# Performance work log

Hardware: AMD Instinct MI355X
Metric: run time of the kernel (lower is better)

Reference implementation:

```python
import jax, jax.numpy as jnp
import numpy as np

N = 100_000      # number of sparse voxels / points
M = 1_000_000    # number of kernel-map (key,query) pairs
C_IN = 128
C_OUT = 128
H = 8            # num_heads
CH = C_OUT // H  # attn_channels = 16
KVOL = 27        # kernel_volume for kernel_size=3, dim=3
EPS_BN = 1e-5
EPS_NORM = 1e-12


def _bn(x, gamma, beta):
    # BatchNorm1d in training mode: batch statistics over point dim
    mu = jnp.mean(x, axis=0)
    var = jnp.var(x, axis=0)
    return (x - mu) * jax.lax.rsqrt(var + EPS_BN) * gamma + beta


def _l2norm(x):
    # F.normalize(p=2, dim=-1) with eps clamp
    n = jnp.sqrt(jnp.sum(x * x, axis=-1, keepdims=True))
    return x / jnp.maximum(n, EPS_NORM)


def setup_inputs() -> dict:
    key = jax.random.key(0)
    ks = jax.random.split(key, 14)
    inp = {
        "points": jax.random.normal(ks[0], (N, 3), jnp.float32),
        "feats": jax.random.normal(ks[1], (N, C_IN), jnp.float32),
        "k_idx": jax.random.randint(ks[2], (M,), 0, N),
        "q_idx": jax.random.randint(ks[3], (M,), 0, N),
        "kernel_idx": jax.random.randint(ks[4], (M,), 0, KVOL),
        # intra_pos_mlp params: Linear(3,3,no bias)-BN-ReLU-Linear(3,C_IN,no bias)-BN-ReLU-Linear(C_IN,C_IN)
        "w1": jax.random.normal(ks[5], (3, 3), jnp.float32) / np.float32(np.sqrt(3.0)),
        "g1": jnp.ones((3,), jnp.float32),
        "b1": jnp.zeros((3,), jnp.float32),
        "w2": jax.random.normal(ks[6], (3, C_IN), jnp.float32) / np.float32(np.sqrt(3.0)),
        "g2": jnp.ones((C_IN,), jnp.float32),
        "b2": jnp.zeros((C_IN,), jnp.float32),
        "w3": jax.random.normal(ks[7], (C_IN, C_IN), jnp.float32) / np.float32(np.sqrt(C_IN)),
        "b3": jnp.zeros((C_IN,), jnp.float32),
        # to_query / to_value (1x1 Minkowski conv == per-point linear) and to_out
        "wq": jax.random.normal(ks[8], (C_IN, C_OUT), jnp.float32) / np.float32(np.sqrt(C_IN)),
        "bq": jnp.zeros((C_OUT,), jnp.float32),
        "wv": jax.random.normal(ks[9], (C_IN, C_OUT), jnp.float32) / np.float32(np.sqrt(C_IN)),
        "bv": jnp.zeros((C_OUT,), jnp.float32),
        "wo": jax.random.normal(ks[10], (C_OUT, C_OUT), jnp.float32) / np.float32(np.sqrt(C_OUT)),
        "bo": jnp.zeros((C_OUT,), jnp.float32),
        # inter_pos_enc ~ N(0,1) per nn.init.normal_
        "pos_enc": jax.random.normal(ks[11], (KVOL, H, CH), jnp.float32),
    }
    return inp


def reference(points, feats, k_idx, q_idx, kernel_idx,
              w1, g1, b1, w2, g2, b2, w3, b3,
              wq, bq, wv, bv, wo, bo, pos_enc):
    # intra positional encoding MLP, added to features
    h = jax.nn.relu(_bn(points @ w1, g1, b1))
    h = jax.nn.relu(_bn(h @ w2, g2, b2))
    x = feats + (h @ w3 + b3)                       # [N, C_IN]
    # per-point query / value projections
    q = (x @ wq + bq).reshape(N, H, CH)             # [N, H, CH]
    v = (x @ wv + bv).reshape(N, H, CH)
    qn = _l2norm(q)
    pn = _l2norm(pos_enc)                           # [KVOL, H, CH]
    # DotProduct op: attn[m,h] = <norm_q[q_idx[m],h], norm_pos_enc[kernel_idx[m],h]>
    attn = jnp.einsum('mhc,mhc->mh', qn[q_idx], pn[kernel_idx])  # [M, H]
    # ScalarAttention op: out[q_idx[m],h,:] += attn[m,h] * v[k_idx[m],h,:]
    out = jnp.zeros((N, H, CH), feats.dtype).at[q_idx].add(attn[:, :, None] * v[k_idx])
    # to_out linear
    return out.reshape(N, C_OUT) @ wo + bo          # [N, C_OUT]
```

## Files before the change

### kernel.cpp

```cpp
#include <hip/hip_runtime.h>
#include <hip/hip_bf16.h>

#define CIN 128
#define NHEAD 8
#define CHD 16
#define KVOL 27
#define NBKT_MAX 512
#define CH 4096
#define NB1 64
#define NB2 256

constexpr float EPS_BN = 1e-5f;
constexpr float EPS_NORM = 1e-12f;

typedef __attribute__((ext_vector_type(8))) short short8;
typedef __attribute__((ext_vector_type(4))) float f32x4;

__device__ __forceinline__ float bflo(unsigned u) {
  return __uint_as_float(u << 16);
}
__device__ __forceinline__ float bfhi(unsigned u) {
  return __uint_as_float(u & 0xffff0000u);
}
__device__ __forceinline__ unsigned pk2bf(float lo, float hi) {
  __hip_bfloat16 a = __float2bfloat16(lo), b = __float2bfloat16(hi);
  return (unsigned)*(unsigned short*)&a | ((unsigned)*(unsigned short*)&b << 16);
}

__global__ __launch_bounds__(256) void k_fuseA(
    const float* __restrict__ points, const float* __restrict__ w1,
    float* __restrict__ partials1, const float* __restrict__ pos_enc,
    const float* __restrict__ wq, const float* __restrict__ wv,
    const float* __restrict__ wo, const float* __restrict__ w3,
    __hip_bfloat16* __restrict__ pnb, __hip_bfloat16* __restrict__ wqT,
    __hip_bfloat16* __restrict__ wvT, __hip_bfloat16* __restrict__ woT,
    __hip_bfloat16* __restrict__ w3b, const int* __restrict__ q_idx,
    int* __restrict__ ccnt, int N, int M) {
  __shared__ __align__(16) char smem[2048];
  int bid = blockIdx.x;
  int t = threadIdx.x;
  if (bid < 64) {
    float(*red)[6] = (float(*)[6])smem;
    float w[9];
#pragma unroll
    for (int i = 0; i < 9; ++i) w[i] = w1[i];
    float s[3] = {0.f, 0.f, 0.f}, ss[3] = {0.f, 0.f, 0.f};
    for (int n = bid * 256 + t; n < N; n += 64 * 256) {
      float p0 = points[3 * n], p1 = points[3 * n + 1], p2 = points[3 * n + 2];
#pragma unroll
      for (int j = 0; j < 3; ++j) {
        float y = p0 * w[j] + p1 * w[3 + j] + p2 * w[6 + j];
        s[j] += y;
        ss[j] += y * y;
      }
    }
#pragma unroll
    for (int j = 0; j < 3; ++j) {
      for (int off = 32; off > 0; off >>= 1) {
        s[j] += __shfl_down(s[j], off);
        ss[j] += __shfl_down(ss[j], off);
      }
    }
    if ((t & 63) == 0) {
      int wv_ = t >> 6;
#pragma unroll
      for (int j = 0; j < 3; ++j) {
        red[wv_][j] = s[j];
        red[wv_][3 + j] = ss[j];
      }
    }
    __syncthreads();
    if (t < 6) {
      float acc = red[0][t] + red[1][t] + red[2][t] + red[3][t];
      partials1[bid * 8 + t] = acc;
    }
  } else if (bid < 128) {
    int g = (bid - 64) * 256 + t;
    if (g < 256) {
      int kk = g >> 3, h = g & 7;
      if (kk < KVOL) {
        const float* src = pos_enc + (kk * NHEAD + h) * CHD;
        float vals[CHD];
        float s = 0.f;
#pragma unroll
        for (int i = 0; i < CHD; ++i) {
          vals[i] = src[i];
          s += vals[i] * vals[i];
        }
        float inv = 1.f / fmaxf(sqrtf(s), EPS_NORM);
#pragma unroll
        for (int i = 0; i < CHD; ++i)
          pnb[kk * CIN + h * CHD + i] = __float2bfloat16(vals[i] * inv);
      } else {
#pragma unroll
        for (int i = 0; i < CHD; ++i)
          pnb[kk * CIN + h * CHD + i] = __float2bfloat16(0.f);
      }
    }
    if (g < CIN * CIN) {
      int k = g >> 7, c = g & 127;
      int gt = c * CIN + k;
      wqT[gt] = __float2bfloat16(wq[g]);
      wvT[gt] = __float2bfloat16(wv[g]);
      woT[gt] = __float2bfloat16(wo[g]);
      w3b[g] = __float2bfloat16(w3[g]);
    }
  } else {
    int* lh = (int*)smem;
    for (int b = t; b < NBKT_MAX; b += 256) lh[b] = 0;
    __syncthreads();
    for (int i = (bid - 128) * 256 + t; i < M; i += 256 * 256)
      atomicAdd(&lh[q_idx[i] >> 8], 1);
    __syncthreads();
    for (int b = t; b < NBKT_MAX; b += 256) {
      int c = lh[b];
      if (c > 0) atomicAdd(&ccnt[b], c);
    }
  }
}

__global__ __launch_bounds__(256) void k_fuseB(
    const float* __restrict__ points, const float* __restrict__ w1,
    const float* __restrict__ g1, const float* __restrict__ b1,
    const float* __restrict__ w2, const float* __restrict__ partials1,
    float* __restrict__ partials2, const int* __restrict__ ccnt,
    int* __restrict__ sbase, int* __restrict__ bcur, int N) {
  __shared__ __align__(16) char smem[3072];
  int t = threadIdx.x;
  if (blockIdx.x < NB2) {
    float(*pa)[3] = (float(*)[3])smem;
    float w[9];
#pragma unroll
    for (int i = 0; i < 9; ++i) w[i] = w1[i];
    float st[6] = {0.f, 0.f, 0.f, 0.f, 0.f, 0.f};
    for (int b = 0; b < NB1; ++b)
#pragma unroll
      for (int j = 0; j < 6; ++j) st[j] += partials1[b * 8 + j];
    float sc1[3], sh1[3];
#pragma unroll
    for (int j = 0; j < 3; ++j) {
      float m = st[j] / (float)N;
      float var = st[3 + j] / (float)N - m * m;
      float sc = rsqrtf(var + EPS_BN) * g1[j];
      sc1[j] = sc;
      sh1[j] = b1[j] - m * sc;
    }
    int c = t & 127, half = t >> 7;
    float wc0 = w2[c], wc1 = w2[CIN + c], wc2 = w2[2 * CIN + c];
    float s = 0.f, ss = 0.f;
    for (int base = blockIdx.x * 256; base < N; base += NB2 * 256) {
      int np = min(256, N - base);
      __syncthreads();
      if (t < np) {
        int n = base + t;
        float p0 = points[3 * n], p1 = points[3 * n + 1],
              p2 = points[3 * n + 2];
        float y0 = p0 * w[0] + p1 * w[3] + p2 * w[6];
        float y1 = p0 * w[1] + p1 * w[4] + p2 * w[7];
        float y2 = p0 * w[2] + p1 * w[5] + p2 * w[8];
        pa[t][0] = fmaxf(y0 * sc1[0] + sh1[0], 0.f);
        pa[t][1] = fmaxf(y1 * sc1[1] + sh1[1], 0.f);
        pa[t][2] = fmaxf(y2 * sc1[2] + sh1[2], 0.f);
      }
      __syncthreads();
      for (int p = half; p < np; p += 2) {
        float y = pa[p][0] * wc0 + pa[p][1] * wc1 + pa[p][2] * wc2;
        s += y;
        ss += y * y;
      }
    }
    __syncthreads();
    float* red = (float*)pa;
    red[t] = s;
    red[256 + t] = ss;
    __syncthreads();
    if (t < 128) {
      partials2[blockIdx.x * CIN + t] = red[t] + red[128 + t];
      partials2[NB2 * CIN + blockIdx.x * CIN + t] =
          red[256 + t] + red[256 + 128 + t];
    }
  } else {
    int* wsum = (int*)smem;
    int s0 = ccnt[2 * t], s1 = ccnt[2 * t + 1];
    int s = s0 + s1;
    int l = t & 63, w = t >> 6;
    int ss = s;
    for (int off = 1; off < 64; off <<= 1) {
      int v = __shfl_up(ss, off);
      if (l >= off) ss += v;
    }
    if (l == 63) wsum[w] = ss;
    __syncthreads();
    int wb = 0;
#pragma unroll
    for (int i = 0; i < 4; ++i)
      if (i < w) wb += wsum[i];
    int ex = wb + ss - s;
    sbase[2 * t] = ex;
    sbase[2 * t + 1] = ex + s0;
    bcur[2 * t] = ex;
    bcur[2 * t + 1] = ex + s0;
    if (t == 255) sbase[NBKT_MAX] = wb + ss;
  }
}

__global__ __launch_bounds__(256) void k_fuseC(
    const float* __restrict__ partials1, const float* __restrict__ partials2,
    float* __restrict__ stats1, float* __restrict__ stats2,
    const __hip_bfloat16* __restrict__ w3b,
    const __hip_bfloat16* __restrict__ wqT,
    const __hip_bfloat16* __restrict__ wvT, const float* __restrict__ wq,
    const float* __restrict__ wv, const float* __restrict__ b3,
    const float* __restrict__ bq, const float* __restrict__ bv,
    __hip_bfloat16* __restrict__ W3qT, __hip_bfloat16* __restrict__ W3vT,
    float* __restrict__ bqp, float* __restrict__ bvp,
    const int* __restrict__ q_idx, const int* __restrict__ k_idx,
    const int* __restrict__ kernel_idx, int* __restrict__ bcur,
    unsigned* __restrict__ stg, int M) {
  __shared__ __align__(16) char smem[22544];
  int bid = blockIdx.x;
  int t = threadIdx.x;
  if (bid == 0) {
    if (t < 128) {
      float s = 0.f, ss = 0.f;
      for (int b = 0; b < NB2; ++b) {
        s += partials2[b * CIN + t];
        ss += partials2[NB2 * CIN + b * CIN + t];
      }
      stats2[t] = s;
      stats2[CIN + t] = ss;
    } else if (t < 134) {
      int j = t - 128;
      float s = 0.f;
      for (int b = 0; b < NB1; ++b) s += partials1[b * 8 + j];
      stats1[j] = s;
    }
  } else if (bid < 6) {
    int pb = bid - 1;
    if (pb == 4) {
      int c = t & 127;
      const float* wsel = (t < 128) ? wq : wv;
      float s = (t < 128) ? bq[c] : bv[c];
      for (int j = 0; j < CIN; ++j) s += b3[j] * wsel[j * CIN + c];
      if (t < 128)
        bqp[c] = s;
      else
        bvp[c] = s;
      return;
    }
    int n0 = pb * 32;
    int w = t >> 6, l = t & 63;
    int lr = l & 15, lg = l >> 4;
    int colbase = w * 32;
    f32x4 cq[2][2], cv[2][2];
#pragma unroll
    for (int mt = 0; mt < 2; ++mt)
#pragma unroll
      for (int nt = 0; nt < 2; ++nt) {
        cq[mt][nt] = {0.f, 0.f, 0.f, 0.f};
        cv[mt][nt] = {0.f, 0.f, 0.f, 0.f};
      }
#pragma unroll
    for (int kk = 0; kk < 4; ++kk) {
      short8 aA[2], bQ[2], bV[2];
#pragma unroll
      for (int mt = 0; mt < 2; ++mt)
        aA[mt] = *(const short8*)(w3b + (size_t)(n0 + mt * 16 + lr) * CIN +
                                  kk * 32 + lg * 8);
#pragma unroll
      for (int nt = 0; nt < 2; ++nt) {
        size_t off = (size_t)(colbase + nt * 16 + lr) * CIN + kk * 32 + lg * 8;
        bQ[nt] = *(const short8*)(wqT + off);
        bV[nt] = *(const short8*)(wvT + off);
      }
#pragma unroll
      for (int mt = 0; mt < 2; ++mt)
#pragma unroll
        for (int nt = 0; nt < 2; ++nt) {
          cq[mt][nt] = __builtin_amdgcn_mfma_f32_16x16x32_bf16(
              aA[mt], bQ[nt], cq[mt][nt], 0, 0, 0);
          cv[mt][nt] = __builtin_amdgcn_mfma_f32_16x16x32_bf16(
              aA[mt], bV[nt], cv[mt][nt], 0, 0, 0);
        }
    }
#pragma unroll
    for (int mt = 0; mt < 2; ++mt)
#pragma unroll
      for (int nt = 0; nt < 2; ++nt)
#pragma unroll
        for (int r = 0; r < 4; ++r) {
          int k = n0 + mt * 16 + lg * 4 + r;
          int c = colbase + nt * 16 + lr;
          W3qT[(size_t)c * CIN + k] = __float2bfloat16(cq[mt][nt][r]);
          W3vT[(size_t)c * CIN + k] = __float2bfloat16(cv[mt][nt][r]);
        }
  } else {
    int* lhist = (int*)smem;
    int* loffs = (int*)(smem + 2048);
    int* lcur = (int*)(smem + 4096);
    int* wsum = (int*)(smem + 6144);
    unsigned* buf = (unsigned*)(smem + 6160);
    int base = (bid - 6) * CH;
    for (int b = t; b < NBKT_MAX; b += 256) lhist[b] = 0;
    __syncthreads();

    int qv_[16];
#pragma unroll
    for (int j = 0; j < 16; ++j) {
      int i = base + t + j * 256;
      int q = (i < M) ? q_idx[i] : -1;
      qv_[j] = q;
      if (q >= 0) atomicAdd(&lhist[q >> 8], 1);
    }
    __syncthreads();

    {
      int s0 = lhist[2 * t], s1 = lhist[2 * t + 1];
      int s = s0 + s1;
      int l = t & 63, w = t >> 6;
      int ss = s;
      for (int off = 1; off < 64; off <<= 1) {
        int v = __shfl_up(ss, off);
        if (l >= off) ss += v;
      }
      if (l == 63) wsum[w] = ss;
      __syncthreads();
      int wb = 0;
#pragma unroll
      for (int i = 0; i < 4; ++i)
        if (i < w) wb += wsum[i];
      int ex = wb + ss - s;
      loffs[2 * t] = ex;
      loffs[2 * t + 1] = ex + s0;
      lcur[2 * t] = ex;
      lcur[2 * t + 1] = ex + s0;
    }
    __syncthreads();

#pragma unroll
    for (int j = 0; j < 16; ++j) {
      int q = qv_[j];
      if (q >= 0) {
        int i = base + t + j * 256;
        unsigned e = (unsigned)k_idx[i] | ((unsigned)kernel_idx[i] << 17) |
                     ((unsigned)(q & 255) << 22);
        int d = atomicAdd(&lcur[q >> 8], 1);
        buf[d] = e;
      }
    }
    __syncthreads();

    for (int b = t; b < NBKT_MAX; b += 256) {
      int cntb = lhist[b];
      if (cntb > 0) {
        int g = atomicAdd(&bcur[b], cntb);
        int lo = loffs[b];
        for (int j = 0; j < cntb; ++j) stg[g + j] = buf[lo + j];
      }
    }
  }
}

__global__ __launch_bounds__(256) void k_bucket2a(
    const unsigned* __restrict__ stg, const int* __restrict__ sbase,
    int* __restrict__ cnt, int N) {
  __shared__ int lh[256];
  int b = blockIdx.x;
  int t = threadIdx.x;
  lh[t] = 0;
  __syncthreads();
  int start = sbase[b];
  int bcnt = sbase[b + 1] - start;
  for (int i = t; i < bcnt; i += 256) atomicAdd(&lh[stg[start + i] >> 22], 1);
  __syncthreads();
  int q = (b << 8) + t;
  if (q < N) cnt[q] = lh[t];
}

__global__ __launch_bounds__(256) void k_scan1(const int* __restrict__ cnt,
                                               int* __restrict__ poffs,
                                               int* __restrict__ bsum, int N) {
  __shared__ int ws_[4];
  int t = threadIdx.x;
  int l = t & 63, w = t >> 6;
  int base = blockIdx.x * 1024 + t * 4;
  int pc[4];
  int s = 0;
#pragma unroll
  for (int j = 0; j < 4; ++j) {
    int c = (base + j < N) ? cnt[base + j] : 0;
    pc[j] = (c + 7) & ~7;
    s += pc[j];
  }
  int own = s;
  for (int off = 1; off < 64; off <<= 1) {
    int v = __shfl_up(s, off);
    if (l >= off) s += v;
  }
  if (l == 63) ws_[w] = s;
  __syncthreads();
  int wbase = 0;
#pragma unroll
  for (int i = 0; i < 4; ++i)
    if (i < w) wbase += ws_[i];
  int ex = wbase + s - own;
#pragma unroll
  for (int j = 0; j < 4; ++j) {
    if (base + j < N) poffs[base + j] = ex;
    ex += pc[j];
  }
  if (t == 255) bsum[blockIdx.x] = wbase + s;
}

__global__ __launch_bounds__(256) void k_scan2(int* __restrict__ bsum,
                                               int* __restrict__ bbase, int NB,
                                               int* __restrict__ poffsN) {
  __shared__ int ws_[4];
  int t = threadIdx.x;
  int l = t & 63, w = t >> 6;
  int s = (t < NB) ? bsum[t] : 0;
  int own = s;
  for (int off = 1; off < 64; off <<= 1) {
    int v = __shfl_up(s, off);
    if (l >= off) s += v;
  }
  if (l == 63) ws_[w] = s;
  __syncthreads();
  int wbase = 0;
#pragma unroll
  for (int i = 0; i < 4; ++i)
    if (i < w) wbase += ws_[i];
  if (t < NB) bbase[t] = wbase + s - own;
  if (t == 255) *poffsN = wbase + s;
}

__global__ __launch_bounds__(256) void k_scan3(const int* __restrict__ cnt,
                                               int* __restrict__ poffs,
                                               const int* __restrict__ bbase,
                                               unsigned* __restrict__ recs,
                                               int N) {
  int t = threadIdx.x;
  int base = blockIdx.x * 1024 + t * 4;
  int bb = bbase[blockIdx.x];
#pragma unroll
  for (int j = 0; j < 4; ++j) {
    int i = base + j;
    if (i >= N) break;
    int o = poffs[i] + bb;
    poffs[i] = o;
    int c = cnt[i];
    int pcend = o + ((c + 7) & ~7);
    for (int p = o + c; p < pcend; ++p) recs[p] = 27u << 17;
  }
}

__global__ __launch_bounds__(256) void k_qv_b2b(
    const unsigned* __restrict__ stg, const int* __restrict__ sbase,
    const int* __restrict__ poffs, unsigned* __restrict__ recs, int NBKT,
    const float* __restrict__ points, const float* __restrict__ feats,
    const float* __restrict__ w1, const float* __restrict__ g1,
    const float* __restrict__ b1, const float* __restrict__ w2,
    const float* __restrict__ g2, const float* __restrict__ b2,
    const __hip_bfloat16* __restrict__ wqT,
    const __hip_bfloat16* __restrict__ wvT,
    const __hip_bfloat16* __restrict__ W3qT,
    const __hip_bfloat16* __restrict__ W3vT, const float* __restrict__ bqp,
    const float* __restrict__ bvp, const float* __restrict__ stats1,
    const float* __restrict__ stats2, __hip_bfloat16* __restrict__ qnout,
    __hip_bfloat16* __restrict__ vout, int N) {
  __shared__ __align__(16) char smem[17792];
  int t = threadIdx.x;
  if ((int)blockIdx.x < NBKT) {
    int* qcur = (int*)smem;
    int b = blockIdx.x;
    int qbase = b << 8;
    int q = qbase + t;
    qcur[t] = (q < N) ? poffs[q] : 0;
    __syncthreads();
    int start = sbase[b];
    int bcnt = sbase[b + 1] - start;
    for (int i = t; i < bcnt; i += 256) {
      unsigned e = stg[start + i];
      int ql = e >> 22;
      unsigned rec = e & 0x3FFFFFu;
      int pos = atomicAdd(&qcur[ql], 1);
      recs[pos] = rec;
    }
    return;
  }
  float(*h0s)[3] = (float(*)[3])smem;
  __hip_bfloat16(*h1s)[136] = (__hip_bfloat16(*)[136])(smem + 384);
  __hip_bfloat16(*fs)[136] = (__hip_bfloat16(*)[136])(smem + 9088);

  int n0 = ((int)blockIdx.x - NBKT) * 32;

  int frow = t >> 3, fpart = t & 7;
  int fn = n0 + frow;
  float4 f0 = {0.f, 0.f, 0.f, 0.f}, f1 = f0, f2 = f0, f3 = f0;
  if (fn < N) {
    const float4* src = (const float4*)(feats + (size_t)fn * CIN + fpart * 16);
    f0 = src[0];
    f1 = src[1];
    f2 = src[2];
    f3 = src[3];
  }

  if (t < 32) {
    int n = n0 + t;
    float p0 = 0.f, p1 = 0.f, p2 = 0.f;
    if (n < N) {
      p0 = points[3 * n];
      p1 = points[3 * n + 1];
      p2 = points[3 * n + 2];
    }
#pragma unroll
    for (int j = 0; j < 3; ++j) {
      float m = stats1[j] / (float)N;
      float var = stats1[3 + j] / (float)N - m * m;
      float sc = rsqrtf(var + EPS_BN) * g1[j];
      float sh = b1[j] - m * sc;
      float y = p0 * w1[j] + p1 * w1[3 + j] + p2 * w1[6 + j];
      h0s[t][j] = fmaxf(y * sc + sh, 0.f);
    }
  }

  {
    unsigned u[8];
    u[0] = pk2bf(f0.x, f0.y);
    u[1] = pk2bf(f0.z, f0.w);
    u[2] = pk2bf(f1.x, f1.y);
    u[3] = pk2bf(f1.z, f1.w);
    u[4] = pk2bf(f2.x, f2.y);
    u[5] = pk2bf(f2.z, f2.w);
    u[6] = pk2bf(f3.x, f3.y);
    u[7] = pk2bf(f3.z, f3.w);
    unsigned* dst = (unsigned*)((char*)&fs[frow][0] + fpart * 32);
#pragma unroll
    for (int i = 0; i < 8; ++i) dst[i] = u[i];
  }
  __syncthreads();

  {
    int c = t & 127, half = t >> 7;
    float m2 = stats2[c] / (float)N;
    float v2 = stats2[CIN + c] / (float)N - m2 * m2;
    float sc2 = rsqrtf(v2 + EPS_BN) * g2[c];
    float sh2 = b2[c] - m2 * sc2;
    float wc0 = w2[c], wc1 = w2[CIN + c], wc2 = w2[2 * CIN + c];
#pragma unroll
    for (int i = 0; i < 16; ++i) {
      int p = i * 2 + half;
      float y = h0s[p][0] * wc0 + h0s[p][1] * wc1 + h0s[p][2] * wc2;
      h1s[p][c] = __float2bfloat16(fmaxf(y * sc2 + sh2, 0.f));
    }
  }
  __syncthreads();

  int w = t >> 6, l = t & 63;
  int lr = l & 15, lg = l >> 4;
  int colbase = w * 32;

  f32x4 aq[2][2], av[2][2];
#pragma unroll
  for (int nt = 0; nt < 2; ++nt) {
    float bqc = bqp[colbase + nt * 16 + lr];
    float bvc = bvp[colbase + nt * 16 + lr];
#pragma unroll
    for (int mt = 0; mt < 2; ++mt) {
      aq[mt][nt] = {bqc, bqc, bqc, bqc};
      av[mt][nt] = {bvc, bvc, bvc, bvc};
    }
  }
#pragma unroll
  for (int kk = 0; kk < 4; ++kk) {
    short8 aF[2], aH[2];
#pragma unroll
    for (int mt = 0; mt < 2; ++mt) {
      aF[mt] = *(const short8*)((const char*)fs + (mt * 16 + lr) * 272 +
                                (kk * 32 + lg * 8) * 2);
      aH[mt] = *(const short8*)((const char*)h1s + (mt * 16 + lr) * 272 +
                                (kk * 32 + lg * 8) * 2);
    }
    short8 bQf[2], bQh[2], bVf[2], bVh[2];
#pragma unroll
    for (int nt = 0; nt < 2; ++nt) {
      size_t off =
          ((size_t)(colbase + nt * 16 + lr) * CIN + kk * 32 + lg * 8) * 2;
      bQf[nt] = *(const short8*)((const char*)wqT + off);
      bQh[nt] = *(const short8*)((const char*)W3qT + off);
      bVf[nt] = *(const short8*)((const char*)wvT + off);
      bVh[nt] = *(const short8*)((const char*)W3vT + off);
    }
#pragma unroll
    for (int mt = 0; mt < 2; ++mt)
#pragma unroll
      for (int nt = 0; nt < 2; ++nt) {
        aq[mt][nt] = __builtin_amdgcn_mfma_f32_16x16x32_bf16(aF[mt], bQf[nt],
                                                             aq[mt][nt], 0, 0, 0);
        aq[mt][nt] = __builtin_amdgcn_mfma_f32_16x16x32_bf16(aH[mt], bQh[nt],
                                                             aq[mt][nt], 0, 0, 0);
        av[mt][nt] = __builtin_amdgcn_mfma_f32_16x16x32_bf16(aF[mt], bVf[nt],
                                                             av[mt][nt], 0, 0, 0);
        av[mt][nt] = __builtin_amdgcn_mfma_f32_16x16x32_bf16(aH[mt], bVh[nt],
                                                             av[mt][nt], 0, 0, 0);
      }
  }
  __syncthreads();

#pragma unroll
  for (int mt = 0; mt < 2; ++mt)
#pragma unroll
    for (int nt = 0; nt < 2; ++nt)
#pragma unroll
      for (int r = 0; r < 4; ++r) {
        float q = aq[mt][nt][r];
        float s = q * q;
        s += __shfl_xor(s, 1);
        s += __shfl_xor(s, 2);
        s += __shfl_xor(s, 4);
        s += __shfl_xor(s, 8);
        float inv = 1.f / fmaxf(sqrtf(s), EPS_NORM);
        int row = mt * 16 + lg * 4 + r;
        int col = colbase + nt * 16 + lr;
        fs[row][col] = __float2bfloat16(q * inv);
        h1s[row][col] = __float2bfloat16(av[mt][nt][r]);
      }
  __syncthreads();

  {
    int row = t >> 3, part = t & 7;
    int n = n0 + row;
    if (n < N) {
      const char* srcq = (const char*)&fs[row][0] + part * 32;
      char* dstq = (char*)qnout + (size_t)n * 256 + part * 32;
      *(uint4*)dstq = *(const uint4*)srcq;
      *(uint4*)(dstq + 16) = *(const uint4*)(srcq + 16);
      const char* srcv = (const char*)&h1s[row][0] + part * 32;
      char* dstv = (char*)vout + (size_t)n * 256 + part * 32;
      *(uint4*)dstv = *(const uint4*)srcv;
      *(uint4*)(dstv + 16) = *(const uint4*)(srcv + 16);
    }
  }
}

__global__ __launch_bounds__(512) void k_gather_out(
    const unsigned* __restrict__ recs, const int* __restrict__ poffs,
    const __hip_bfloat16* __restrict__ qn, const __hip_bfloat16* __restrict__ v,
    const __hip_bfloat16* __restrict__ pnb,
    const __hip_bfloat16* __restrict__ woT, const float* __restrict__ bo,
    float* __restrict__ out, int N) {
  __shared__ __hip_bfloat16 accs[32][136];
  __shared__ float dotlds[32][224];
  int t = threadIdx.x;
  int w = t >> 6, l = t & 63;
  int h = l >> 3;
  int n0 = blockIdx.x * 32;
  const char* vbase = (const char*)v + 4 * l;

  {
    int row = t >> 4, part = t & 15;
    int n = n0 + row;
    uint4 val = {0u, 0u, 0u, 0u};
    if (n < N)
      val = *(const uint4*)((const char*)qn + (size_t)n * 256 + part * 16);
    *(uint4*)((char*)&accs[row][0] + part * 16) = val;
  }
  __syncthreads();

  {
    int lr = l & 15, lg = l >> 4;
    int rg = w & 1;
    const short8 zero8 = {0, 0, 0, 0, 0, 0, 0, 0};
#pragma unroll
    for (int hh = 0; hh < 2; ++hh) {
      int hx = (w >> 1) * 2 + hh;
      short8 aA = zero8, bB0 = zero8, bB1 = zero8;
      if (lg < 2) {
        aA = *(const short8*)((const char*)&accs[rg * 16 + lr][0] +
                              (hx * CHD + lg * 8) * 2);
        bB0 = *(const short8*)(pnb + lr * CIN + hx * CHD + lg * 8);
        bB1 = *(const short8*)(pnb + (16 + lr) * CIN + hx * CHD + lg * 8);
      }
      f32x4 c0 = {0.f, 0.f, 0.f, 0.f}, c1 = {0.f, 0.f, 0.f, 0.f};
      c0 = __builtin_amdgcn_mfma_f32_16x16x32_bf16(aA, bB0, c0, 0, 0, 0);
      c1 = __builtin_amdgcn_mfma_f32_16x16x32_bf16(aA, bB1, c1, 0, 0, 0);
#pragma unroll
      for (int r = 0; r < 4; ++r) {
        int row = rg * 16 + lg * 4 + r;
        dotlds[row][lr * 8 + hx] = c0[r];
        if (lr < 12) dotlds[row][(16 + lr) * 8 + hx] = c1[r];
      }
    }
  }
  __syncthreads();

#pragma unroll 1
  for (int j = 0; j < 4; ++j) {
    int nl = w * 4 + j;
    int n = n0 + nl;
    float ax = 0.f, ay = 0.f;
    if (n < N) {
      const float* dptr = &dotlds[nl][0];
      int beg = poffs[n], end = poffs[n + 1];
      for (int idx = beg; idx < end; idx += 8) {
        unsigned r0 = recs[idx + 0], r1 = recs[idx + 1], r2 = recs[idx + 2],
                 r3 = recs[idx + 3], r4 = recs[idx + 4], r5 = recs[idx + 5],
                 r6 = recs[idx + 6], r7 = recs[idx + 7];
        unsigned v0 = *(const unsigned*)(vbase + (size_t)(r0 & 0x1FFFF) * 256);
        unsigned v1 = *(const unsigned*)(vbase + (size_t)(r1 & 0x1FFFF) * 256);
        unsigned v2 = *(const unsigned*)(vbase + (size_t)(r2 & 0x1FFFF) * 256);
        unsigned v3 = *(const unsigned*)(vbase + (size_t)(r3 & 0x1FFFF) * 256);
        unsigned v4 = *(const unsigned*)(vbase + (size_t)(r4 & 0x1FFFF) * 256);
        unsigned v5 = *(const unsigned*)(vbase + (size_t)(r5 & 0x1FFFF) * 256);
        unsigned v6 = *(const unsigned*)(vbase + (size_t)(r6 & 0x1FFFF) * 256);
        unsigned v7 = *(const unsigned*)(vbase + (size_t)(r7 & 0x1FFFF) * 256);
        float a0 = dptr[(r0 >> 17) * 8 + h];
        float a1 = dptr[(r1 >> 17) * 8 + h];
        float a2 = dptr[(r2 >> 17) * 8 + h];
        float a3 = dptr[(r3 >> 17) * 8 + h];
        float a4 = dptr[(r4 >> 17) * 8 + h];
        float a5 = dptr[(r5 >> 17) * 8 + h];
        float a6 = dptr[(r6 >> 17) * 8 + h];
        float a7 = dptr[(r7 >> 17) * 8 + h];
        ax += a0 * bflo(v0);
        ay += a0 * bfhi(v0);
        ax += a1 * bflo(v1);
        ay += a1 * bfhi(v1);
        ax += a2 * bflo(v2);
        ay += a2 * bfhi(v2);
        ax += a3 * bflo(v3);
        ay += a3 * bfhi(v3);
        ax += a4 * bflo(v4);
        ay += a4 * bfhi(v4);
        ax += a5 * bflo(v5);
        ay += a5 * bfhi(v5);
        ax += a6 * bflo(v6);
        ay += a6 * bfhi(v6);
        ax += a7 * bflo(v7);
        ay += a7 * bfhi(v7);
      }
    }
    __hip_bfloat16 bx = __float2bfloat16(ax), by = __float2bfloat16(ay);
    unsigned pk = (unsigned)*(unsigned short*)&bx |
                  ((unsigned)*(unsigned short*)&by << 16);
    ((unsigned*)((char*)accs + nl * 272))[l] = pk;
  }
  __syncthreads();

  int lr = l & 15, lg = l >> 4;
  int colb = w * 16;
  float bc = bo[colb + lr];
  f32x4 acc0 = {bc, bc, bc, bc}, acc1 = {bc, bc, bc, bc};
#pragma unroll
  for (int kk = 0; kk < 4; ++kk) {
    short8 aA0 = *(const short8*)((const char*)accs + lr * 272 +
                                  (kk * 32 + lg * 8) * 2);
    short8 aA1 = *(const short8*)((const char*)accs + (16 + lr) * 272 +
                                  (kk * 32 + lg * 8) * 2);
    short8 bB = *(const short8*)(woT + (size_t)(colb + lr) * CIN + kk * 32 +
                                 lg * 8);
    acc0 = __builtin_amdgcn_mfma_f32_16x16x32_bf16(aA0, bB, acc0, 0, 0, 0);
    acc1 = __builtin_amdgcn_mfma_f32_16x16x32_bf16(aA1, bB, acc1, 0, 0, 0);
  }
#pragma unroll
  for (int r = 0; r < 4; ++r) {
    int nr0 = n0 + lg * 4 + r;
    int nr1 = nr0 + 16;
    if (nr0 < N) out[(size_t)nr0 * CIN + colb + lr] = acc0[r];
    if (nr1 < N) out[(size_t)nr1 * CIN + colb + lr] = acc1[r];
  }
}

extern "C" void kernel_launch(void* const* d_in, const int* in_sizes, int n_in,
                              void* d_out, int out_size, void* d_ws,
                              size_t ws_size, hipStream_t stream) {
  const float* points = (const float*)d_in[0];
  const float* feats = (const float*)d_in[1];
  const int* k_idx = (const int*)d_in[2];
  const int* q_idx = (const int*)d_in[3];
  const int* kernel_idx = (const int*)d_in[4];
  const float* w1 = (const float*)d_in[5];
  const float* g1 = (const float*)d_in[6];
  const float* b1 = (const float*)d_in[7];
  const float* w2 = (const float*)d_in[8];
  const float* g2 = (const float*)d_in[9];
  const float* b2 = (const float*)d_in[10];
  const float* w3 = (const float*)d_in[11];
  const float* b3 = (const float*)d_in[12];
  const float* wq = (const float*)d_in[13];
  const float* bq = (const float*)d_in[14];
  const float* wv = (const float*)d_in[15];
  const float* bv = (const float*)d_in[16];
  const float* wo = (const float*)d_in[17];
  const float* bo = (const float*)d_in[18];
  const float* pos_enc = (const float*)d_in[19];

  int N = in_sizes[0] / 3;
  int M = in_sizes[2];
  int NB = (N + 1023) / 1024;
  int NBKT = (N + 255) >> 8;
  int Np = (N + 4) & ~3;
  int NB1C = (M + CH - 1) / CH;

  float* ws = (float*)d_ws;
  float* stats1 = ws;
  float* stats2 = ws + 8;
  __hip_bfloat16* pnb = (__hip_bfloat16*)(ws + 264);
  float* bqp = ws + 2312;
  float* bvp = ws + 2440;
  int* cnt = (int*)(ws + 4096);
  int* poffs = cnt + Np;
  int* bsum = poffs + Np;
  int* bbase = bsum + 512;
  int* bcur = bbase + 512;
  int* ccnt = bcur + 512;
  int* sbase = ccnt + 512;
  unsigned* recs = (unsigned*)(sbase + 520);
  size_t recn = ((size_t)M + 8 * (size_t)N + 7) & ~(size_t)7;
  unsigned* stg = recs + recn;
  __hip_bfloat16* qnb = (__hip_bfloat16*)(stg + M);
  __hip_bfloat16* vb = qnb + (size_t)N * CIN;
  __hip_bfloat16* wqT = vb + (size_t)N * CIN;
  __hip_bfloat16* wvT = wqT + CIN * CIN;
  __hip_bfloat16* woT = wvT + CIN * CIN;
  __hip_bfloat16* W3qT = woT + CIN * CIN;
  __hip_bfloat16* W3vT = W3qT + CIN * CIN;
  __hip_bfloat16* w3b = W3vT + CIN * CIN;
  float* partials1 = (float*)(w3b + CIN * CIN);
  float* partials2 = partials1 + NB1 * 8;
  float* outf = (float*)d_out;

  hipMemsetAsync(ccnt, 0, NBKT_MAX * sizeof(int), stream);

  k_fuseA<<<384, 256, 0, stream>>>(points, w1, partials1, pos_enc, wq, wv, wo,
                                   w3, pnb, wqT, wvT, woT, w3b, q_idx, ccnt, N,
                                   M);
  k_fuseB<<<NB2 + 1, 256, 0, stream>>>(points, w1, g1, b1, w2, partials1,
                                       partials2, ccnt, sbase, bcur, N);
  k_fuseC<<<6 + NB1C, 256, 0, stream>>>(partials1, partials2, stats1, stats2,
                                        w3b, wqT, wvT, wq, wv, b3, bq, bv, W3qT,
                                        W3vT, bqp, bvp, q_idx, k_idx,
                                        kernel_idx, bcur, stg, M);
  k_bucket2a<<<NBKT, 256, 0, stream>>>(stg, sbase, cnt, N);
  k_scan1<<<NB, 256, 0, stream>>>(cnt, poffs, bsum, N);
  k_scan2<<<1, 256, 0, stream>>>(bsum, bbase, NB, poffs + N);
  k_scan3<<<NB, 256, 0, stream>>>(cnt, poffs, bbase, recs, N);
  k_qv_b2b<<<NBKT + (N + 31) / 32, 256, 0, stream>>>(
      stg, sbase, poffs, recs, NBKT, points, feats, w1, g1, b1, w2, g2, b2, wqT,
      wvT, W3qT, W3vT, bqp, bvp, stats1, stats2, qnb, vb, N);
  k_gather_out<<<(N + 31) / 32, 512, 0, stream>>>(recs, poffs, qnb, vb, pnb,
                                                  woT, bo, outf, N);
}
```

Baseline: 219.7 us.

## Fuse bucket histogram into scan1, use rsqrt normalize, head-major dot LDS layout

Merges the per-bucket histogram kernel into the first scan kernel: each scan block counts four buckets directly into shared memory and scans those counts, removing one launch and the global round trip of the counts. The L2 normalization now uses rsqrt of the clamped squared norm instead of a divide by sqrt. The dot-product table in LDS is re-laid out head-major (stride 28 per head), so the gather loop reads contiguous kernel-offset entries for a fixed head, which may change bank-conflict behaviour. The fused kernel does more atomic work per block, which lowers parallelism in that stage.

```diff
diff --git a/kernel.cpp b/kernel.cpp
--- a/kernel.cpp
+++ b/kernel.cpp
@@ -361,34 +361,35 @@
   }
 }
 
-__global__ __launch_bounds__(256) void k_bucket2a(
+__global__ __launch_bounds__(256) void k_scan1(
     const unsigned* __restrict__ stg, const int* __restrict__ sbase,
-    int* __restrict__ cnt, int N) {
-  __shared__ int lh[256];
-  int b = blockIdx.x;
-  int t = threadIdx.x;
-  lh[t] = 0;
-  __syncthreads();
-  int start = sbase[b];
-  int bcnt = sbase[b + 1] - start;
-  for (int i = t; i < bcnt; i += 256) atomicAdd(&lh[stg[start + i] >> 22], 1);
-  __syncthreads();
-  int q = (b << 8) + t;
-  if (q < N) cnt[q] = lh[t];
-}
-
-__global__ __launch_bounds__(256) void k_scan1(const int* __restrict__ cnt,
-                                               int* __restrict__ poffs,
-                                               int* __restrict__ bsum, int N) {
+    int* __restrict__ cnt, int* __restrict__ poffs, int* __restrict__ bsum,
+    int N) {
+  __shared__ int lh[1024];
   __shared__ int ws_[4];
   int t = threadIdx.x;
+  int b = blockIdx.x;
+  for (int i = t; i < 1024; i += 256) lh[i] = 0;
+  __syncthreads();
+#pragma unroll
+  for (int sb = 0; sb < 4; ++sb) {
+    int bkt = b * 4 + sb;
+    int s0 = sbase[bkt], s1 = sbase[bkt + 1];
+    for (int i = s0 + t; i < s1; i += 256)
+      atomicAdd(&lh[sb * 256 + (stg[i] >> 22)], 1);
+  }
+  __syncthreads();
   int l = t & 63, w = t >> 6;
-  int base = blockIdx.x * 1024 + t * 4;
+  int base = b * 1024 + t * 4;
   int pc[4];
   int s = 0;
 #pragma unroll
   for (int j = 0; j < 4; ++j) {
-    int c = (base + j < N) ? cnt[base + j] : 0;
+    int c = lh[t * 4 + j];
+    if (base + j < N)
+      cnt[base + j] = c;
+    else
+      c = 0;
     pc[j] = (c + 7) & ~7;
     s += pc[j];
   }
@@ -409,7 +410,7 @@
     if (base + j < N) poffs[base + j] = ex;
     ex += pc[j];
   }
-  if (t == 255) bsum[blockIdx.x] = wbase + s;
+  if (t == 255) bsum[b] = wbase + s;
 }
 
 __global__ __launch_bounds__(256) void k_scan2(int* __restrict__ bsum,
@@ -619,7 +620,7 @@
         s += __shfl_xor(s, 2);
         s += __shfl_xor(s, 4);
         s += __shfl_xor(s, 8);
-        float inv = 1.f / fmaxf(sqrtf(s), EPS_NORM);
+        float inv = rsqrtf(fmaxf(s, EPS_NORM * EPS_NORM));
         int row = mt * 16 + lg * 4 + r;
         int col = colbase + nt * 16 + lr;
         fs[row][col] = __float2bfloat16(q * inv);
@@ -687,13 +688,14 @@
 #pragma unroll
       for (int r = 0; r < 4; ++r) {
         int row = rg * 16 + lg * 4 + r;
-        dotlds[row][lr * 8 + hx] = c0[r];
-        if (lr < 12) dotlds[row][(16 + lr) * 8 + hx] = c1[r];
-      }
-    }
-  }
-  __syncthreads();
-
+        dotlds[row][hx * 28 + lr] = c0[r];
+        if (lr < 12) dotlds[row][hx * 28 + 16 + lr] = c1[r];
+      }
+    }
+  }
+  __syncthreads();
+
+  int hb = h * 28;
 #pragma unroll 1
   for (int j = 0; j < 4; ++j) {
     int nl = w * 4 + j;
@@ -714,14 +716,14 @@
         unsigned v5 = *(const unsigned*)(vbase + (size_t)(r5 & 0x1FFFF) * 256);
         unsigned v6 = *(const unsigned*)(vbase + (size_t)(r6 & 0x1FFFF) * 256);
         unsigned v7 = *(const unsigned*)(vbase + (size_t)(r7 & 0x1FFFF) * 256);
-        float a0 = dptr[(r0 >> 17) * 8 + h];
-        float a1 = dptr[(r1 >> 17) * 8 + h];
-        float a2 = dptr[(r2 >> 17) * 8 + h];
-        float a3 = dptr[(r3 >> 17) * 8 + h];
-        float a4 = dptr[(r4 >> 17) * 8 + h];
-        float a5 = dptr[(r5 >> 17) * 8 + h];
-        float a6 = dptr[(r6 >> 17) * 8 + h];
-        float a7 = dptr[(r7 >> 17) * 8 + h];
+        float a0 = dptr[hb + (r0 >> 17)];
+        float a1 = dptr[hb + (r1 >> 17)];
+        float a2 = dptr[hb + (r2 >> 17)];
+        float a3 = dptr[hb + (r3 >> 17)];
+        float a4 = dptr[hb + (r4 >> 17)];
+        float a5 = dptr[hb + (r5 >> 17)];
+        float a6 = dptr[hb + (r6 >> 17)];
+        float a7 = dptr[hb + (r7 >> 17)];
         ax += a0 * bflo(v0);
         ay += a0 * bfhi(v0);
         ax += a1 * bflo(v1);
@@ -841,8 +843,7 @@
                                         w3b, wqT, wvT, wq, wv, b3, bq, bv, W3qT,
                                         W3vT, bqp, bvp, q_idx, k_idx,
                                         kernel_idx, bcur, stg, M);
-  k_bucket2a<<<NBKT, 256, 0, stream>>>(stg, sbase, cnt, N);
-  k_scan1<<<NB, 256, 0, stream>>>(cnt, poffs, bsum, N);
+  k_scan1<<<NB, 256, 0, stream>>>(stg, sbase, cnt, poffs, bsum, N);
   k_scan2<<<1, 256, 0, stream>>>(bsum, bbase, NB, poffs + N);
   k_scan3<<<NB, 256, 0, stream>>>(cnt, poffs, bbase, recs, N);
   k_qv_b2b<<<NBKT + (N + 31) / 32, 256, 0, stream>>>(
```

New measurement: 223.8 us. About the same (+1.8%).
